# Kernel tuning notes

Measured on AMD Instinct MI355X. Metric: run time of the kernel, lower is better.

## Reference

```python
import jax, jax.numpy as jnp
import numpy as np

MAX_CHILD = 64  # max trie branching factor (padding width for per-row child windows)


def setup_inputs() -> dict:
    key = jax.random.key(0)
    B, D, V, N = 1024, 1024, 32000, 200000
    k1, k2, k3, k4 = jax.random.split(key, 4)
    x = jax.random.normal(k1, (B, D), dtype=jnp.float32)
    weight = jax.random.normal(k2, (V, D), dtype=jnp.float32) * 0.02
    bias = jax.random.normal(k3, (V,), dtype=jnp.float32) * 0.02
    # Build a consistent CompactCSRTrie: offsets [N+1], tokens/child_nodes [E]
    rng = np.random.default_rng(0)
    deg = rng.integers(1, MAX_CHILD + 1, size=N)
    offsets = np.zeros(N + 1, dtype=np.int32)
    offsets[1:] = np.cumsum(deg)
    E = int(offsets[-1])
    tokens = rng.integers(0, V, size=E).astype(np.int32)
    child_nodes = rng.integers(0, N, size=E).astype(np.int32)
    cur_node = jax.random.randint(k4, (B,), 0, N, dtype=jnp.int32)
    return {
        "x": x,
        "weight": weight,
        "bias": bias,
        "cur_node": cur_node,
        "offsets": jnp.asarray(offsets),
        "tokens": jnp.asarray(tokens),
        "child_nodes": jnp.asarray(child_nodes),
        "step": 1,
    }


def reference(x, weight, bias, cur_node, offsets, tokens, child_nodes, step):
    # Dense GEMM part of the fused kernel: logits = x @ W^T + b  -> [B, V]
    logits = jnp.einsum("bd,vd->bv", x, weight) + bias
    B, V = logits.shape

    # CSR trie traversal: per row, the children of cur_node are
    # tokens[offsets[cur]:offsets[cur+1]] (valid next tokens) and
    # child_nodes[...] (next trie nodes). Gather a padded MAX_CHILD window.
    start = offsets[cur_node]                              # [B]
    deg = offsets[cur_node + 1] - start                    # [B]
    pos = jnp.arange(MAX_CHILD, dtype=start.dtype)         # [C]
    idx = jnp.minimum(start[:, None] + pos[None, :], tokens.shape[0] - 1)  # [B, C]
    valid = pos[None, :] < deg[:, None]                    # [B, C] bool

    tok = tokens[idx]                                      # [B, C] valid token columns
    child = child_nodes[idx]                               # [B, C] next trie nodes

    # Validity masking: only valid child tokens keep their logit, rest -> -inf
    rows = jnp.arange(B)[:, None]
    mask = jnp.zeros((B, V), dtype=bool).at[rows, tok].max(valid)
    masked_logits = jnp.where(mask, logits, -jnp.inf)

    next_nodes = jnp.where(valid, child, -1)               # [B, C], -1 padded
    valid_idxs = jnp.where(valid, tok, -1)                 # [B, C], -1 padded
    return next_nodes, valid_idxs, masked_logits
```

## Files before the change

### kernel.cpp

```cpp
#include <hip/hip_runtime.h>
#include <math.h>

#define B_ 1024
#define D_ 1024
#define V_ 32000
#define MAXC 64

#define NEG_FILL (-3.0e38f)

typedef float vfloat4 __attribute__((ext_vector_type(4)));

__global__ __launch_bounds__(256, 4) void fill_compute_kernel(
    const float* __restrict__ x,
    const float* __restrict__ weight,
    const float* __restrict__ bias,
    const int* __restrict__ cur_node,
    const int* __restrict__ offsets,
    const int* __restrict__ tokens,
    float* __restrict__ out)
{
    const int bid = blockIdx.x;
    const int b = bid >> 2;
    const int q = bid & 3;
    const int tid = threadIdx.x;
    const int wave = tid >> 6;
    const int lane = tid & 63;

    const int cur = cur_node[b];
    const int start = offsets[cur];
    int deg = offsets[cur + 1] - start;
    if (deg > MAXC) deg = MAXC;

    const float4* x4 = reinterpret_cast<const float4*>(x + (size_t)b * D_);
    float4 xv[4];
    #pragma unroll
    for (int k = 0; k < 4; ++k)
        xv[k] = x4[k * 64 + lane];

    float4 wv[4][4];
    float bj[4];
    #pragma unroll
    for (int j = 0; j < 4; ++j) {
        const int c = q * 16 + wave * 4 + j;
        if (c < deg) {
            const int t = tokens[start + c];
            bj[j] = bias[t];
            const float4* w4 = reinterpret_cast<const float4*>(weight + (size_t)t * D_);
            #pragma unroll
            for (int k = 0; k < 4; ++k)
                wv[j][k] = w4[k * 64 + lane];
        }
    }

    vfloat4* ml4 = reinterpret_cast<vfloat4*>(out + 2 * (size_t)B_ * MAXC + (size_t)b * V_);
    const vfloat4 sent = {NEG_FILL, NEG_FILL, NEG_FILL, NEG_FILL};
    const int qbase = q * (V_ / 16);
    #pragma unroll 2
    for (int i = qbase + tid; i < qbase + V_ / 16; i += 256)
        __builtin_nontemporal_store(sent, &ml4[i]);

    float* vals = out;
    #pragma unroll
    for (int j = 0; j < 4; ++j) {
        const int c = q * 16 + wave * 4 + j;
        if (c < deg) {
            float acc = 0.0f;
            #pragma unroll
            for (int k = 0; k < 4; ++k)
                acc += wv[j][k].x * xv[k].x + wv[j][k].y * xv[k].y +
                       wv[j][k].z * xv[k].z + wv[j][k].w * xv[k].w;
            #pragma unroll
            for (int off = 32; off > 0; off >>= 1)
                acc += __shfl_xor(acc, off);
            if (lane == 0)
                vals[b * MAXC + c] = acc + bj[j];
        }
    }
}

__global__ __launch_bounds__(256) void scatter_kernel(
    const int* __restrict__ cur_node,
    const int* __restrict__ offsets,
    const int* __restrict__ tokens,
    const int* __restrict__ child_nodes,
    float* __restrict__ out)
{
    const int gid = blockIdx.x * 256 + threadIdx.x;
    const int b = gid >> 6;
    const int c = gid & (MAXC - 1);

    const int cur = cur_node[b];
    const int start = offsets[cur];
    int deg = offsets[cur + 1] - start;
    if (deg > MAXC) deg = MAXC;

    float nn = -1.0f, vi = -1.0f;
    if (c < deg) {
        const int e = start + c;
        const int tok = tokens[e];
        const float val = out[gid];
        out[2 * (size_t)B_ * MAXC + (size_t)b * V_ + tok] = val;
        nn = (float)child_nodes[e];
        vi = (float)tok;
    }
    out[gid] = nn;
    out[(size_t)B_ * MAXC + gid] = vi;
}

extern "C" void kernel_launch(void* const* d_in, const int* in_sizes, int n_in,
                              void* d_out, int out_size, void* d_ws, size_t ws_size,
                              hipStream_t stream) {
    const float* x           = (const float*)d_in[0];
    const float* weight      = (const float*)d_in[1];
    const float* bias        = (const float*)d_in[2];
    const int*   cur_node    = (const int*)d_in[3];
    const int*   offsets     = (const int*)d_in[4];
    const int*   tokens      = (const int*)d_in[5];
    const int*   child_nodes = (const int*)d_in[6];

    float* out = (float*)d_out;

    fill_compute_kernel<<<B_ * 4, 256, 0, stream>>>(
        x, weight, bias, cur_node, offsets, tokens, out);
    scatter_kernel<<<(B_ * MAXC) / 256, 256, 0, stream>>>(
        cur_node, offsets, tokens, child_nodes, out);
}
```

Before: 54.41 us.

## Split fill and gather into separate block roles with double-buffered weight loads

```diff
diff --git a/kernel.cpp b/kernel.cpp
--- a/kernel.cpp
+++ b/kernel.cpp
@@ -5,12 +5,17 @@
 #define D_ 1024
 #define V_ 32000
 #define MAXC 64
+#define HDR (2 * B_ * MAXC)
+#define LOGF4 ((B_ * V_) / 4)
+#define NGATHER 1024
+#define NFILL 2048
+#define FILL_F4 4096
 
 #define NEG_FILL (-3.0e38f)
 
 typedef float vfloat4 __attribute__((ext_vector_type(4)));
 
-__global__ __launch_bounds__(256, 4) void fill_compute_kernel(
+__global__ __launch_bounds__(256, 8) void fill_gather_kernel(
     const float* __restrict__ x,
     const float* __restrict__ weight,
     const float* __restrict__ bias,
@@ -20,9 +25,22 @@
     float* __restrict__ out)
 {
     const int bid = blockIdx.x;
-    const int b = bid >> 2;
-    const int q = bid & 3;
     const int tid = threadIdx.x;
+
+    if (bid >= NGATHER) {
+        vfloat4* ml4 = reinterpret_cast<vfloat4*>(out + HDR);
+        const vfloat4 sent = {NEG_FILL, NEG_FILL, NEG_FILL, NEG_FILL};
+        const int base = (bid - NGATHER) * FILL_F4 + tid;
+        #pragma unroll
+        for (int j = 0; j < FILL_F4 / 256; ++j) {
+            const int i = base + j * 256;
+            if (i < LOGF4)
+                __builtin_nontemporal_store(sent, &ml4[i]);
+        }
+        return;
+    }
+
+    const int b    = bid;
     const int wave = tid >> 6;
     const int lane = tid & 63;
 
@@ -37,45 +55,69 @@
     for (int k = 0; k < 4; ++k)
         xv[k] = x4[k * 64 + lane];
 
-    float4 wv[4][4];
-    float bj[4];
-    #pragma unroll
-    for (int j = 0; j < 4; ++j) {
-        const int c = q * 16 + wave * 4 + j;
-        if (c < deg) {
-            const int t = tokens[start + c];
-            bj[j] = bias[t];
+    const int sbase = wave * 16;
+    int cnt = deg - sbase;
+    if (cnt < 0) cnt = 0;
+    if (cnt > 16) cnt = 16;
+
+    int tok = 0;
+    float bv = 0.0f;
+    if (lane < 16 && sbase + lane < deg) {
+        tok = tokens[start + sbase + lane];
+        bv = bias[tok];
+    }
+
+    float myval = 0.0f;
+    float4 wA[4], wB[4];
+    if (cnt > 0) {
+        const int t0 = __shfl(tok, 0);
+        const float4* w4 = reinterpret_cast<const float4*>(weight + (size_t)t0 * D_);
+        #pragma unroll
+        for (int k = 0; k < 4; ++k) wA[k] = w4[k * 64 + lane];
+    }
+    int i = 0;
+    while (i < cnt) {
+        if (i + 1 < cnt) {
+            const int t = __shfl(tok, i + 1);
             const float4* w4 = reinterpret_cast<const float4*>(weight + (size_t)t * D_);
             #pragma unroll
-            for (int k = 0; k < 4; ++k)
-                wv[j][k] = w4[k * 64 + lane];
+            for (int k = 0; k < 4; ++k) wB[k] = w4[k * 64 + lane];
         }
-    }
-
-    vfloat4* ml4 = reinterpret_cast<vfloat4*>(out + 2 * (size_t)B_ * MAXC + (size_t)b * V_);
-    const vfloat4 sent = {NEG_FILL, NEG_FILL, NEG_FILL, NEG_FILL};
-    const int qbase = q * (V_ / 16);
-    #pragma unroll 2
-    for (int i = qbase + tid; i < qbase + V_ / 16; i += 256)
-        __builtin_nontemporal_store(sent, &ml4[i]);
-
-    float* vals = out;
-    #pragma unroll
-    for (int j = 0; j < 4; ++j) {
-        const int c = q * 16 + wave * 4 + j;
-        if (c < deg) {
+        {
             float acc = 0.0f;
             #pragma unroll
             for (int k = 0; k < 4; ++k)
-                acc += wv[j][k].x * xv[k].x + wv[j][k].y * xv[k].y +
-                       wv[j][k].z * xv[k].z + wv[j][k].w * xv[k].w;
+                acc += wA[k].x * xv[k].x + wA[k].y * xv[k].y +
+                       wA[k].z * xv[k].z + wA[k].w * xv[k].w;
             #pragma unroll
             for (int off = 32; off > 0; off >>= 1)
                 acc += __shfl_xor(acc, off);
-            if (lane == 0)
-                vals[b * MAXC + c] = acc + bj[j];
+            if (lane == i) myval = acc + bv;
         }
+        ++i;
+        if (i >= cnt) break;
+        if (i + 1 < cnt) {
+            const int t = __shfl(tok, i + 1);
+            const float4* w4 = reinterpret_cast<const float4*>(weight + (size_t)t * D_);
+            #pragma unroll
+            for (int k = 0; k < 4; ++k) wA[k] = w4[k * 64 + lane];
+        }
+        {
+            float acc = 0.0f;
+            #pragma unroll
+            for (int k = 0; k < 4; ++k)
+                acc += wB[k].x * xv[k].x + wB[k].y * xv[k].y +
+                       wB[k].z * xv[k].z + wB[k].w * xv[k].w;
+            #pragma unroll
+            for (int off = 32; off > 0; off >>= 1)
+                acc += __shfl_xor(acc, off);
+            if (lane == i) myval = acc + bv;
+        }
+        ++i;
     }
+
+    if (lane < 16 && sbase + lane < deg)
+        out[b * MAXC + sbase + lane] = myval;
 }
 
 __global__ __launch_bounds__(256) void scatter_kernel(
@@ -99,7 +141,7 @@
         const int e = start + c;
         const int tok = tokens[e];
         const float val = out[gid];
-        out[2 * (size_t)B_ * MAXC + (size_t)b * V_ + tok] = val;
+        out[HDR + (size_t)b * V_ + tok] = val;
         nn = (float)child_nodes[e];
         vi = (float)tok;
     }
@@ -120,7 +162,7 @@
 
     float* out = (float*)d_out;
 
-    fill_compute_kernel<<<B_ * 4, 256, 0, stream>>>(
+    fill_gather_kernel<<<NGATHER + NFILL, 256, 0, stream>>>(
         x, weight, bias, cur_node, offsets, tokens, out);
     scatter_kernel<<<(B_ * MAXC) / 256, 256, 0, stream>>>(
         cur_node, offsets, tokens, child_nodes, out);
```

Result: slower. 57.31 us (+5.3%).

## Group trie children by token to reuse weight rows across batch rows

Applied to the files above, without the earlier changes.

```diff
diff --git a/kernel.cpp b/kernel.cpp
--- a/kernel.cpp
+++ b/kernel.cpp
@@ -8,87 +8,118 @@
 
 #define NEG_FILL (-3.0e38f)
 
+#define CAP 16
+#define MAGIC_BITS 0x7FC0DEAD
+#define TAB_OFF 32768
+#define CV_OFF (TAB_OFF + V_ * CAP)
+
+#define NSB 2000
+#define NFB 2048
+#define LOGF4 ((B_ * V_) / 4)
+
 typedef float vfloat4 __attribute__((ext_vector_type(4)));
 
-__global__ __launch_bounds__(256, 4) void fill_compute_kernel(
+__global__ __launch_bounds__(256) void k0_zero(int* __restrict__ wsi)
+{
+    const int i = blockIdx.x * 256 + threadIdx.x;
+    if (i < V_) wsi[i] = 0;
+}
+
+__global__ __launch_bounds__(256) void k1_build(
+    const int* __restrict__ cur_node,
+    const int* __restrict__ offsets,
+    const int* __restrict__ tokens,
+    int* __restrict__ wsi,
+    float* __restrict__ wsf)
+{
+    const int gid = blockIdx.x * 256 + threadIdx.x;
+    const int b = gid >> 6, c = gid & (MAXC - 1);
+    const int cur = cur_node[b];
+    const int start = offsets[cur];
+    int deg = offsets[cur + 1] - start;
+    if (deg > MAXC) deg = MAXC;
+    if (c >= deg) return;
+    const int tok = tokens[start + c];
+    const int slot = atomicAdd(&wsi[tok], 1);
+    if (slot < CAP)
+        wsi[TAB_OFF + tok * CAP + slot] = gid;
+    else
+        wsf[CV_OFF + gid] = __int_as_float(MAGIC_BITS);
+}
+
+__global__ __launch_bounds__(256, 8) void k2_main(
+    const float* __restrict__ x,
+    const float* __restrict__ weight,
+    const float* __restrict__ bias,
+    const int* __restrict__ wsi,
+    float* __restrict__ wsf,
+    float* __restrict__ masked_logits)
+{
+    const int bid = blockIdx.x;
+    const int tid = threadIdx.x;
+
+    if (bid >= NSB) {
+        vfloat4* ml4 = reinterpret_cast<vfloat4*>(masked_logits);
+        const vfloat4 sent = {NEG_FILL, NEG_FILL, NEG_FILL, NEG_FILL};
+        const int base = (bid - NSB) * 4096 + tid;
+        #pragma unroll
+        for (int j = 0; j < 16; ++j) {
+            const int i = base + j * 256;
+            if (i < LOGF4)
+                __builtin_nontemporal_store(sent, &ml4[i]);
+        }
+        return;
+    }
+
+    const int wave = tid >> 6, lane = tid & 63;
+    const float4* w4 = reinterpret_cast<const float4*>(weight);
+    const float4* x4 = reinterpret_cast<const float4*>(x);
+
+    for (int r = 0; r < 4; ++r) {
+        const int v = bid * 16 + wave * 4 + r;
+        const int cnt = wsi[v];
+        if (cnt == 0) continue;
+        const size_t vb = (size_t)v * 256;
+        const float4 wv0 = w4[vb + 0 * 64 + lane];
+        const float4 wv1 = w4[vb + 1 * 64 + lane];
+        const float4 wv2 = w4[vb + 2 * 64 + lane];
+        const float4 wv3 = w4[vb + 3 * 64 + lane];
+        const float bv = bias[v];
+        const int m = cnt < CAP ? cnt : CAP;
+        for (int j = 0; j < m; ++j) {
+            const int e = wsi[TAB_OFF + v * CAP + j];
+            const int b = e >> 6;
+            const size_t xb = (size_t)b * 256;
+            const float4 xv0 = x4[xb + 0 * 64 + lane];
+            const float4 xv1 = x4[xb + 1 * 64 + lane];
+            const float4 xv2 = x4[xb + 2 * 64 + lane];
+            const float4 xv3 = x4[xb + 3 * 64 + lane];
+            float acc = wv0.x * xv0.x + wv0.y * xv0.y + wv0.z * xv0.z + wv0.w * xv0.w;
+            acc      += wv1.x * xv1.x + wv1.y * xv1.y + wv1.z * xv1.z + wv1.w * xv1.w;
+            acc      += wv2.x * xv2.x + wv2.y * xv2.y + wv2.z * xv2.z + wv2.w * xv2.w;
+            acc      += wv3.x * xv3.x + wv3.y * xv3.y + wv3.z * xv3.z + wv3.w * xv3.w;
+            #pragma unroll
+            for (int off = 32; off > 0; off >>= 1)
+                acc += __shfl_xor(acc, off);
+            if (lane == 0)
+                wsf[CV_OFF + e] = acc + bv;
+        }
+    }
+}
+
+__global__ __launch_bounds__(256) void k3_final(
     const float* __restrict__ x,
     const float* __restrict__ weight,
     const float* __restrict__ bias,
     const int* __restrict__ cur_node,
     const int* __restrict__ offsets,
     const int* __restrict__ tokens,
-    float* __restrict__ out)
-{
-    const int bid = blockIdx.x;
-    const int b = bid >> 2;
-    const int q = bid & 3;
-    const int tid = threadIdx.x;
-    const int wave = tid >> 6;
-    const int lane = tid & 63;
-
-    const int cur = cur_node[b];
-    const int start = offsets[cur];
-    int deg = offsets[cur + 1] - start;
-    if (deg > MAXC) deg = MAXC;
-
-    const float4* x4 = reinterpret_cast<const float4*>(x + (size_t)b * D_);
-    float4 xv[4];
-    #pragma unroll
-    for (int k = 0; k < 4; ++k)
-        xv[k] = x4[k * 64 + lane];
-
-    float4 wv[4][4];
-    float bj[4];
-    #pragma unroll
-    for (int j = 0; j < 4; ++j) {
-        const int c = q * 16 + wave * 4 + j;
-        if (c < deg) {
-            const int t = tokens[start + c];
-            bj[j] = bias[t];
-            const float4* w4 = reinterpret_cast<const float4*>(weight + (size_t)t * D_);
-            #pragma unroll
-            for (int k = 0; k < 4; ++k)
-                wv[j][k] = w4[k * 64 + lane];
-        }
-    }
-
-    vfloat4* ml4 = reinterpret_cast<vfloat4*>(out + 2 * (size_t)B_ * MAXC + (size_t)b * V_);
-    const vfloat4 sent = {NEG_FILL, NEG_FILL, NEG_FILL, NEG_FILL};
-    const int qbase = q * (V_ / 16);
-    #pragma unroll 2
-    for (int i = qbase + tid; i < qbase + V_ / 16; i += 256)
-        __builtin_nontemporal_store(sent, &ml4[i]);
-
-    float* vals = out;
-    #pragma unroll
-    for (int j = 0; j < 4; ++j) {
-        const int c = q * 16 + wave * 4 + j;
-        if (c < deg) {
-            float acc = 0.0f;
-            #pragma unroll
-            for (int k = 0; k < 4; ++k)
-                acc += wv[j][k].x * xv[k].x + wv[j][k].y * xv[k].y +
-                       wv[j][k].z * xv[k].z + wv[j][k].w * xv[k].w;
-            #pragma unroll
-            for (int off = 32; off > 0; off >>= 1)
-                acc += __shfl_xor(acc, off);
-            if (lane == 0)
-                vals[b * MAXC + c] = acc + bj[j];
-        }
-    }
-}
-
-__global__ __launch_bounds__(256) void scatter_kernel(
-    const int* __restrict__ cur_node,
-    const int* __restrict__ offsets,
-    const int* __restrict__ tokens,
     const int* __restrict__ child_nodes,
+    const float* __restrict__ wsf,
     float* __restrict__ out)
 {
     const int gid = blockIdx.x * 256 + threadIdx.x;
-    const int b = gid >> 6;
-    const int c = gid & (MAXC - 1);
-
+    const int b = gid >> 6, c = gid & (MAXC - 1);
     const int cur = cur_node[b];
     const int start = offsets[cur];
     int deg = offsets[cur + 1] - start;
@@ -98,7 +129,13 @@
     if (c < deg) {
         const int e = start + c;
         const int tok = tokens[e];
-        const float val = out[gid];
+        float val = wsf[CV_OFF + gid];
+        if (__float_as_int(val) == MAGIC_BITS) {
+            float acc = 0.0f;
+            for (int k = 0; k < D_; ++k)
+                acc += x[b * D_ + k] * weight[(size_t)tok * D_ + k];
+            val = acc + bias[tok];
+        }
         out[2 * (size_t)B_ * MAXC + (size_t)b * V_ + tok] = val;
         nn = (float)child_nodes[e];
         vi = (float)tok;
@@ -119,9 +156,15 @@
     const int*   child_nodes = (const int*)d_in[6];
 
     float* out = (float*)d_out;
+    float* masked_logits = out + 2 * (size_t)B_ * MAXC;
+    int*   wsi = (int*)d_ws;
+    float* wsf = (float*)d_ws;
 
-    fill_compute_kernel<<<B_ * 4, 256, 0, stream>>>(
-        x, weight, bias, cur_node, offsets, tokens, out);
-    scatter_kernel<<<(B_ * MAXC) / 256, 256, 0, stream>>>(
-        cur_node, offsets, tokens, child_nodes, out);
+    k0_zero<<<(V_ + 255) / 256, 256, 0, stream>>>(wsi);
+    k1_build<<<(B_ * MAXC) / 256, 256, 0, stream>>>(
+        cur_node, offsets, tokens, wsi, wsf);
+    k2_main<<<NSB + NFB, 256, 0, stream>>>(
+        x, weight, bias, wsi, wsf, masked_logits);
+    k3_final<<<(B_ * MAXC) / 256, 256, 0, stream>>>(
+        x, weight, bias, cur_node, offsets, tokens, child_nodes, wsf, out);
 }
```

Measured after the change: 58.95 us. 8.3% more time.
